# Optimization experiments

Hardware: AMD Instinct MI355X
Metric: run time of the kernel (lower is better)

Reference implementation:

```python
import jax, jax.numpy as jnp
import numpy as np

B, DX, DY, H, K = 16384, 128, 128, 2048, 16
MIN_BIN = 1e-3   # min bin width/height (nflows convention)
MIN_DERIV = 1e-3  # min knot derivative


def setup_inputs() -> dict:
    key = jax.random.key(0)
    k0, k1, k2, k3 = jax.random.split(key, 4)
    x = jax.random.normal(k0, (B, DX), jnp.float32)
    y = jax.random.uniform(k1, (B, DY), jnp.float32, minval=1e-4, maxval=1.0 - 1e-4)
    W1 = jax.random.normal(k2, (DX, H), jnp.float32) / np.sqrt(DX).astype(np.float32)
    b1 = jnp.zeros((H,), jnp.float32)
    W2 = jax.random.normal(k3, (H, DY * (3 * K + 1)), jnp.float32) / np.sqrt(H).astype(np.float32)
    b2 = jnp.zeros((DY * (3 * K + 1),), jnp.float32)
    return {"x": x, "y": y, "W1": W1, "b1": b1, "W2": W2, "b2": b2}


def _rq_spline(y, pdf):
    # y: [B, D] in (0,1); pdf: [B, D, 3K+1] unnormalized spline params
    w_un, h_un, d_un = pdf[..., :K], pdf[..., K:2 * K], pdf[..., 2 * K:]
    widths = MIN_BIN + (1.0 - K * MIN_BIN) * jax.nn.softmax(w_un, axis=-1)   # [B,D,K]
    heights = MIN_BIN + (1.0 - K * MIN_BIN) * jax.nn.softmax(h_un, axis=-1)  # [B,D,K]
    derivs = MIN_DERIV + jax.nn.softplus(d_un)                               # [B,D,K+1]

    pad = [(0, 0), (0, 0), (1, 0)]
    cw = jnp.pad(jnp.cumsum(widths, axis=-1), pad)    # knot x-positions [B,D,K+1]
    ch = jnp.pad(jnp.cumsum(heights, axis=-1), pad)   # knot y-positions [B,D,K+1]

    # data-dependent bin lookup (searchsorted equivalent, vectorized)
    idx = jnp.clip(jnp.sum(y[..., None] >= cw, axis=-1) - 1, 0, K - 1)  # [B,D]
    g = lambda a: jnp.take_along_axis(a, idx[..., None], axis=-1)[..., 0]
    xk, yk = g(cw), g(ch)
    wk, hk = g(widths), g(heights)
    dk = g(derivs)
    dk1 = jnp.take_along_axis(derivs, idx[..., None] + 1, axis=-1)[..., 0]

    s = hk / wk                      # bin slope
    t = (y - xk) / wk                # theta in [0,1]
    omt = 1.0 - t
    denom = s + (dk1 + dk - 2.0 * s) * t * omt
    out = yk + hk * (s * t * t + dk * t * omt) / denom
    deriv = s * s * (dk1 * t * t + 2.0 * s * t * omt + dk * omt * omt) / (denom * denom)
    dlogp = jnp.sum(jnp.log(deriv), axis=-1, keepdims=True)  # [B,1]
    return out, dlogp


def reference(x, y, W1, b1, W2, b2):
    # conditioner MLP: x -> spline params
    h = jax.nn.relu(x @ W1 + b1)
    pdf = (h @ W2 + b2).reshape(x.shape[0], DY, 3 * K + 1)
    return _rq_spline(y, pdf)
```

## Files before the change

kernel.cpp:

```cpp
#include <hip/hip_runtime.h>
#include <hip/hip_fp16.h>
#include <cstdint>
#include <cstddef>

#define B_ROWS 16384
#define DX 128
#define DYDIM 128
#define HDIM 2048
#define NPARAM 49
#define NCOL 6272
#define NTILES 26
#define W2PROWS (NTILES * 256)

typedef __attribute__((ext_vector_type(8))) _Float16 half8v;
typedef __attribute__((ext_vector_type(4))) float f32x4;

__global__ void k_f32_to_f16(const float* __restrict__ in, _Float16* __restrict__ out, int n) {
  int i = blockIdx.x * 256 + threadIdx.x;
  if (i < n) out[i] = (_Float16)in[i];
}

__global__ void k_transpose_f16(const float* __restrict__ in, _Float16* __restrict__ out, int R, int C) {
  __shared__ float tile[32][33];
  int c0 = blockIdx.x * 32, r0 = blockIdx.y * 32;
  int tx = threadIdx.x;
  for (int i = threadIdx.y; i < 32; i += 8)
    tile[i][tx] = in[(size_t)(r0 + i) * C + c0 + tx];
  __syncthreads();
  for (int i = threadIdx.y; i < 32; i += 8)
    out[(size_t)(c0 + i) * R + r0 + tx] = (_Float16)tile[tx][i];
}

__global__ void k_transpose_perm(const float* __restrict__ in, _Float16* __restrict__ out) {
  __shared__ float tile[32][33];
  int c0 = blockIdx.x * 32, r0 = blockIdx.y * 32;
  int tx = threadIdx.x;
  for (int i = threadIdx.y; i < 32; i += 8)
    tile[i][tx] = in[(size_t)(r0 + i) * NCOL + c0 + tx];
  __syncthreads();
  for (int i = threadIdx.y; i < 32; i += 8) {
    int g = c0 + i;
    int t = g / 245;
    int cc = g - t * 245;
    out[(size_t)(t * 256 + cc) * HDIM + r0 + tx] = (_Float16)tile[tx][i];
  }
}

__global__ __launch_bounds__(256) void k_gemm1(
    const _Float16* __restrict__ A, const _Float16* __restrict__ Bt,
    const float* __restrict__ bias, _Float16* __restrict__ C,
    int M, int N, int K) {
  __shared__ _Float16 Abuf[128 * 32];
  __shared__ _Float16 Bbuf[128 * 32];
  const int t = threadIdx.x;
  const int l = t & 63;
  const int w = t >> 6;
  int bx = blockIdx.x, by = blockIdx.y;
  {
    const int nx = gridDim.x;
    const int nwg = nx * gridDim.y;
    const int lin = by * nx + bx;
    const int cpx = nwg >> 3;
    const int sw = (lin & 7) * cpx + (lin >> 3);
    bx = sw % nx;
    by = sw / nx;
  }
  const int tileM = by * 128;
  const int tileN = bx * 128;
  const int wm = w >> 1, wn = w & 1;
  const int srow = w * 16 + (l >> 2);
  const int skel = (l & 3) * 8;
  const char* Ag = (const char*)(A + (size_t)(tileM + srow) * K + skel);
  const char* Bg = (const char*)(Bt + (size_t)(tileN + srow) * K + skel);
  const size_t gRowStep = (size_t)64 * K * 2;
  auto ldsA = (__attribute__((address_space(3))) char*)Abuf;
  auto ldsB = (__attribute__((address_space(3))) char*)Bbuf;
  const int ldsBase = w * 1024;
  f32x4 acc[4][4];
#pragma unroll
  for (int i = 0; i < 4; ++i)
#pragma unroll
    for (int j = 0; j < 4; ++j) acc[i][j] = (f32x4){0.f, 0.f, 0.f, 0.f};
  const int nk = K >> 5;
#define STAGE1(kt)                                                                             \
  do {                                                                                         \
    size_t koff = (size_t)(kt) * 64;                                                           \
    __builtin_amdgcn_global_load_lds(                                                          \
        (const __attribute__((address_space(1))) uint32_t*)(Ag + koff),                        \
        (__attribute__((address_space(3))) uint32_t*)(ldsA + ldsBase), 16, 0, 0);              \
    __builtin_amdgcn_global_load_lds(                                                          \
        (const __attribute__((address_space(1))) uint32_t*)(Ag + koff + gRowStep),             \
        (__attribute__((address_space(3))) uint32_t*)(ldsA + 4096 + ldsBase), 16, 0, 0);       \
    __builtin_amdgcn_global_load_lds(                                                          \
        (const __attribute__((address_space(1))) uint32_t*)(Bg + koff),                        \
        (__attribute__((address_space(3))) uint32_t*)(ldsB + ldsBase), 16, 0, 0);              \
    __builtin_amdgcn_global_load_lds(                                                          \
        (const __attribute__((address_space(1))) uint32_t*)(Bg + koff + gRowStep),             \
        (__attribute__((address_space(3))) uint32_t*)(ldsB + 4096 + ldsBase), 16, 0, 0);       \
  } while (0)
  STAGE1(0);
  const int abase = (wm * 64 + (l & 15)) * 32 + (l >> 4) * 8;
  const int bbase = (wn * 64 + (l & 15)) * 32 + (l >> 4) * 8;
  for (int kt = 0; kt < nk; ++kt) {
    __syncthreads();
    half8v av[4], bv[4];
#pragma unroll
    for (int mf = 0; mf < 4; ++mf)
      av[mf] = *(const half8v*)((const _Float16*)Abuf + abase + mf * 512);
#pragma unroll
    for (int nf = 0; nf < 4; ++nf)
      bv[nf] = *(const half8v*)((const _Float16*)Bbuf + bbase + nf * 512);
#pragma unroll
    for (int mf = 0; mf < 4; ++mf)
#pragma unroll
      for (int nf = 0; nf < 4; ++nf)
        acc[mf][nf] = __builtin_amdgcn_mfma_f32_16x16x32_f16(av[mf], bv[nf], acc[mf][nf], 0, 0, 0);
    __syncthreads();
    if (kt + 1 < nk) STAGE1(kt + 1);
  }
#undef STAGE1
  const int crow0 = tileM + wm * 64 + (l >> 4) * 4;
  const int ccol0 = tileN + wn * 64 + (l & 15);
#pragma unroll
  for (int nf = 0; nf < 4; ++nf) {
    const int col = ccol0 + nf * 16;
    const float bvv = bias[col];
#pragma unroll
    for (int mf = 0; mf < 4; ++mf) {
#pragma unroll
      for (int j = 0; j < 4; ++j) {
        const int row = crow0 + mf * 16 + j;
        float v = fmaxf(acc[mf][nf][j] + bvv, 0.f);
        C[(size_t)row * N + col] = (_Float16)v;
      }
    }
  }
}

__global__ __launch_bounds__(512, 2) void k_gemm2s(
    const _Float16* __restrict__ A, const _Float16* __restrict__ Bt,
    const float* __restrict__ bias, const float* __restrict__ y,
    float* __restrict__ outp, float* __restrict__ gpart, int M) {
  constexpr int K = HDIM;
  constexpr int K2 = K * 2;
  constexpr int NT = K / 64;
  constexpr int ITERS = NT / 2;

  __shared__ char smem[131072];
  __shared__ float red[512];

  const int t = threadIdx.x;
  const int l = t & 63;
  const int w = t >> 6;
  const int wm = w >> 2;
  const int wn = w & 3;
  const int rlo = l & 15;
  const int khi = l >> 4;
  const int wOff = w * 1024;

  int bx = blockIdx.x, by = blockIdx.y;
  {
    const int nx = gridDim.x;
    const int nwg = nx * gridDim.y;
    const int lin = by * nx + bx;
    const int cpx = nwg >> 3;
    const int sw = (lin & 7) * cpx + (lin >> 3);
    bx = sw % nx;
    by = sw / nx;
  }
  const int tileM = by * 256;
  const int tileN = bx * 256;

  int rowj[2], kbj[2];
#pragma unroll
  for (int j = 0; j < 2; ++j) {
    const int phys = j * 8192 + t * 16;
    const int b = phys ^ (((phys >> 9) & 1) << 5);
    rowj[j] = ((b >> 11) << 4) + ((b >> 6) & 15);
    kbj[j] = (((b >> 10) & 1) << 6) + (b & 63);
  }
  const char* pA[2][2];
  const char* pB[2][2];
#pragma unroll
  for (int half = 0; half < 2; ++half)
#pragma unroll
    for (int j = 0; j < 2; ++j) {
      pA[half][j] = (const char*)A + (size_t)(tileM + half * 128 + rowj[j]) * K2 + kbj[j];
      pB[half][j] = (const char*)Bt + (size_t)(tileN + half * 128 + rowj[j]) * K2 + kbj[j];
    }

  auto lds3 = (__attribute__((address_space(3))) char*)smem;

#define LDSA(d, half) ((d) * 32768 + (half) * 16384)
#define LDSB(d, half) (65536 + (d) * 32768 + (half) * 16384)
#define GLDS(srcp, ldsoff)                                                                   \
  __builtin_amdgcn_global_load_lds(                                                           \
      (const __attribute__((address_space(1))) uint32_t*)(srcp),                              \
      (__attribute__((address_space(3))) uint32_t*)(lds3 + (ldsoff) + wOff), 16, 0, 0)
#define STG(op, d, half, kt)                                                                  \
  do {                                                                                        \
    GLDS(p##op[half][0] + (size_t)(kt) * 128, LDS##op(d, half));                              \
    GLDS(p##op[half][1] + (size_t)(kt) * 128, LDS##op(d, half) + 8192);                       \
  } while (0)
#define VM(n) asm volatile("s_waitcnt vmcnt(" #n ")" ::: "memory")
#define NOSTG ((void)0)
#define NOW ((void)0)
#define CFENCE asm volatile("" ::: "memory")

  const int swz = (rlo & 8) ? 32 : 0;
  const int lane16 = rlo * 64 + ((khi * 16) ^ swz);
  const int aW = wm * 8192 + lane16;
  const int bW = 65536 + wn * 4096 + lane16;

  half8v b000, b001, b010, b011, b100, b101, b110, b111;
  f32x4 acc[8][4];
#pragma unroll
  for (int i = 0; i < 8; ++i)
#pragma unroll
    for (int j = 0; j < 4; ++j) acc[i][j] = (f32x4){0.f, 0.f, 0.f, 0.f};

#define MF(fi, gj, av, bv) \
  acc[fi][gj] = __builtin_amdgcn_mfma_f32_16x16x32_f16(av, bv, acc[fi][gj], 0, 0, 0)

#define PHX(d, q, LOADB, WAITS, ...)                                                          \
  do {                                                                                        \
    const int aB = (d) * 32768 + ((q) >> 1) * 16384 + ((q) & 1) * 4096 + aW;                  \
    half8v a00 = *(const half8v*)(smem + aB);                                                 \
    half8v a01 = *(const half8v*)(smem + aB + 1024);                                          \
    half8v a10 = *(const half8v*)(smem + aB + 2048);                                          \
    half8v a11 = *(const half8v*)(smem + aB + 3072);                                          \
    if (LOADB) {                                                                              \
      const int bB = (d) * 32768 + bW;                                                        \
      b000 = *(const half8v*)(smem + bB);                                                     \
      b001 = *(const half8v*)(smem + bB + 1024);                                              \
      b010 = *(const half8v*)(smem + bB + 2048);                                              \
      b011 = *(const half8v*)(smem + bB + 3072);                                              \
      b100 = *(const half8v*)(smem + bB + 16384);                                             \
      b101 = *(const half8v*)(smem + bB + 17408);                                             \
      b110 = *(const half8v*)(smem + bB + 18432);                                             \
      b111 = *(const half8v*)(smem + bB + 19456);                                             \
    }                                                                                         \
    __VA_ARGS__;                                                                              \
    WAITS;                                                                                    \
    CFENCE;                                                                                   \
    __builtin_amdgcn_s_barrier();                                                             \
    CFENCE;                                                                                   \
    __builtin_amdgcn_s_setprio(1);                                                            \
    {                                                                                         \
      constexpr int f0 = ((q) >> 1) * 4 + ((q) & 1) * 2;                                      \
      MF(f0 + 0, 0, a00, b000); MF(f0 + 0, 0, a01, b001);                                     \
      MF(f0 + 0, 1, a00, b010); MF(f0 + 0, 1, a01, b011);                                     \
      MF(f0 + 0, 2, a00, b100); MF(f0 + 0, 2, a01, b101);                                     \
      MF(f0 + 0, 3, a00, b110); MF(f0 + 0, 3, a01, b111);                                     \
      MF(f0 + 1, 0, a10, b000); MF(f0 + 1, 0, a11, b001);                                     \
      MF(f0 + 1, 1, a10, b010); MF(f0 + 1, 1, a11, b011);                                     \
      MF(f0 + 1, 2, a10, b100); MF(f0 + 1, 2, a11, b101);                                     \
      MF(f0 + 1, 3, a10, b110); MF(f0 + 1, 3, a11, b111);                                     \
    }                                                                                         \
    __builtin_amdgcn_s_setprio(0);                                                            \
    CFENCE;                                                                                   \
    __builtin_amdgcn_s_barrier();                                                             \
  } while (0)

  STG(B, 0, 0, 0);
  STG(B, 0, 1, 0);
  STG(A, 0, 0, 0);
  STG(A, 0, 1, 0);
  STG(B, 1, 0, 1);
  STG(B, 1, 1, 1);
  STG(A, 1, 0, 1);
  VM(6);
  CFENCE;
  __builtin_amdgcn_s_barrier();

  for (int it = 0; it < ITERS - 1; ++it) {
    const int kt = 2 * it;
    PHX(0, 0, 1, NOW, STG(A, 1, 1, kt + 1));
    PHX(0, 1, 0, NOW, STG(B, 0, 0, kt + 2));
    PHX(0, 2, 0, NOW, STG(B, 0, 1, kt + 2); STG(A, 0, 0, kt + 2));
    PHX(0, 3, 0, VM(8), NOSTG);
    PHX(1, 0, 1, NOW, STG(A, 0, 1, kt + 2));
    PHX(1, 1, 0, VM(10), STG(B, 1, 0, kt + 3));
    PHX(1, 2, 0, NOW, STG(B, 1, 1, kt + 3); STG(A, 1, 0, kt + 3));
    PHX(1, 3, 0, VM(6), NOSTG);
  }
  PHX(0, 0, 1, NOW, STG(A, 1, 1, NT - 1));
  PHX(0, 1, 0, NOW, NOSTG);
  PHX(0, 2, 0, NOW, NOSTG);
  PHX(0, 3, 0, VM(2), NOSTG);
  PHX(1, 0, 1, NOW, NOSTG);
  PHX(1, 1, 0, VM(0), NOSTG);
  PHX(1, 2, 0, NOW, NOSTG);
  PHX(1, 3, 0, NOW, NOSTG);

#undef PHX
#undef MF
#undef STG
#undef GLDS
#undef LDSA
#undef LDSB

  const int RCt = (bx < 25) ? 245 : 147;
  const int nd  = (bx < 25) ? 5 : 3;

#pragma unroll
  for (int fi = 0; fi < 8; ++fi) {
    const int r0l = (((fi >> 2) * 2 + wm) << 6) + ((fi & 3) << 4) + khi * 4;
#pragma unroll
    for (int gj = 0; gj < 4; ++gj) {
      const int c = (((gj >> 1) * 4 + wn) << 5) + ((gj & 1) << 4) + rlo;
      if (c < RCt) {
        const float bvv = bias[245 * bx + c];
#pragma unroll
        for (int j = 0; j < 4; ++j) {
          const int r = r0l + j;
          *(_Float16*)(smem + r * 512 + ((2 * c) ^ ((r & 31) << 4))) =
              (_Float16)(acc[fi][gj][j] + bvv);
        }
      }
    }
  }
  __syncthreads();

  float lsum = 0.f;
#pragma unroll
  for (int pass = 0; pass < 3; ++pass) {
    const int task = pass * 512 + t;
    const int d = task >> 8;
    const int r = task & 255;
    if (d < nd) {
      const int rbase = r * 512;
      const int rswz = (r & 31) << 4;
      const int cb = 2 * (d * 49);
#define LQ(j) ((float)*(const _Float16*)(smem + rbase + ((cb + 2 * (j)) ^ rswz)))
      float mw = -1e30f, mh = -1e30f;
#pragma unroll
      for (int j = 0; j < 16; ++j) {
        mw = fmaxf(mw, LQ(j));
        mh = fmaxf(mh, LQ(16 + j));
      }
      float sw2 = 0.f, sh = 0.f;
#pragma unroll
      for (int j = 0; j < 16; ++j) {
        sw2 += __expf(LQ(j) - mw);
        sh += __expf(LQ(16 + j) - mh);
      }
      const float rw = 0.984f / sw2, rh = 0.984f / sh;
      const int rg = tileM + r;
      const int dg = 5 * bx + d;
      const float yv = y[(size_t)rg * DYDIM + dg];

      float cws = 0.f, chs = 0.f, xk = 0.f, yk = 0.f, wk = 1.f, hk = 1.f;
      int idx = 0;
#pragma unroll
      for (int j = 0; j < 16; ++j) {
        float wj = 0.001f + rw * __expf(LQ(j) - mw);
        float hj = 0.001f + rh * __expf(LQ(16 + j) - mh);
        if (yv >= cws) { idx = j; xk = cws; yk = chs; wk = wj; hk = hj; }
        cws += wj;
        chs += hj;
      }
      const float du0 = LQ(32 + idx), du1 = LQ(33 + idx);
      const float dk  = 0.001f + fmaxf(du0, 0.f) + log1pf(__expf(-fabsf(du0)));
      const float dk1 = 0.001f + fmaxf(du1, 0.f) + log1pf(__expf(-fabsf(du1)));

      const float s = hk / wk;
      const float tt = (yv - xk) / wk;
      const float omt = 1.f - tt;
      const float dnm = s + (dk1 + dk - 2.f * s) * tt * omt;
      const float o = yk + hk * (s * tt * tt + dk * tt * omt) / dnm;
      const float dr = s * s * (dk1 * tt * tt + 2.f * s * tt * omt + dk * omt * omt) / (dnm * dnm);

      outp[(size_t)rg * DYDIM + dg] = o;
      lsum += __logf(dr);
#undef LQ
    }
  }
  red[t] = lsum;
  __syncthreads();
  if (t < 256)
    gpart[(size_t)bx * B_ROWS + (tileM + t)] = red[t] + red[t + 256];
}

__global__ void k_dlogp_reduce(const float* __restrict__ gpart, float* __restrict__ dlogp) {
  int b = blockIdx.x * 256 + threadIdx.x;
  float s = 0.f;
  for (int tt = 0; tt < NTILES; ++tt) s += gpart[(size_t)tt * B_ROWS + b];
  dlogp[b] = s;
}

extern "C" void kernel_launch(void* const* d_in, const int* in_sizes, int n_in,
                              void* d_out, int out_size, void* d_ws, size_t ws_size,
                              hipStream_t stream) {
  const float* x  = (const float*)d_in[0];
  const float* y  = (const float*)d_in[1];
  const float* W1 = (const float*)d_in[2];
  const float* b1 = (const float*)d_in[3];
  const float* W2 = (const float*)d_in[4];
  const float* b2 = (const float*)d_in[5];
  float* out = (float*)d_out;
  float* dlogp = out + (size_t)B_ROWS * DYDIM;

  char* ws = (char*)d_ws;
  _Float16* w2p = (_Float16*)ws;
  _Float16* h   = w2p + (size_t)W2PROWS * HDIM;
  _Float16* xb  = h + (size_t)B_ROWS * HDIM;
  _Float16* w1t = xb + (size_t)B_ROWS * DX;
  float* gpart  = (float*)(w1t + (size_t)HDIM * DX);

  k_f32_to_f16<<<(B_ROWS * DX + 255) / 256, 256, 0, stream>>>(x, xb, B_ROWS * DX);
  k_transpose_f16<<<dim3(HDIM / 32, DX / 32), dim3(32, 8), 0, stream>>>(W1, w1t, DX, HDIM);
  k_transpose_perm<<<dim3(NCOL / 32, HDIM / 32), dim3(32, 8), 0, stream>>>(W2, w2p);

  k_gemm1<<<dim3(HDIM / 128, B_ROWS / 128), 256, 0, stream>>>(
      xb, w1t, b1, h, B_ROWS, HDIM, DX);

  k_gemm2s<<<dim3(NTILES, B_ROWS / 256), 512, 0, stream>>>(
      h, w2p, b2, y, out, gpart, B_ROWS);

  k_dlogp_reduce<<<B_ROWS / 256, 256, 0, stream>>>(gpart, dlogp);
}
```

Measured before the change: 502.7 us.

## Transpose epilogue LDS layout, remap XCD tile order, reorder MFMA issue

Stores the biased GEMM2 output tile into LDS column-major with packed 32-bit half pairs, so each thread reading a spline parameter column hits consecutive rows across lanes. Spline parameters are loaded once into registers, which removes the repeated LDS reads for the softmax max, sum and bin search, and the y loads are hoisted ahead of the loop. The workgroup-to-tile mapping is hardcoded so each XCD gets 8 contiguous row tiles for L2 reuse, and the MFMA issue order is changed to reuse A fragments. Holding the parameters in registers raises register pressure, and the hardcoded mapping assumes the exact 26x64 grid.

New measurement: 489.9 us. 1.03x faster.

```diff
diff --git a/kernel.cpp b/kernel.cpp
--- a/kernel.cpp
+++ b/kernel.cpp
@@ -160,13 +160,11 @@
 
   int bx = blockIdx.x, by = blockIdx.y;
   {
-    const int nx = gridDim.x;
-    const int nwg = nx * gridDim.y;
-    const int lin = by * nx + bx;
-    const int cpx = nwg >> 3;
-    const int sw = (lin & 7) * cpx + (lin >> 3);
-    bx = sw % nx;
-    by = sw / nx;
+    const int lin = by * 26 + bx;
+    const int xcd = lin & 7;
+    const int slot = lin >> 3;
+    bx = slot >> 3;
+    by = xcd * 8 + (slot & 7);
   }
   const int tileM = by * 256;
   const int tileN = bx * 256;
@@ -248,14 +246,14 @@
     __builtin_amdgcn_s_setprio(1);                                                            \
     {                                                                                         \
       constexpr int f0 = ((q) >> 1) * 4 + ((q) & 1) * 2;                                      \
-      MF(f0 + 0, 0, a00, b000); MF(f0 + 0, 0, a01, b001);                                     \
-      MF(f0 + 0, 1, a00, b010); MF(f0 + 0, 1, a01, b011);                                     \
-      MF(f0 + 0, 2, a00, b100); MF(f0 + 0, 2, a01, b101);                                     \
-      MF(f0 + 0, 3, a00, b110); MF(f0 + 0, 3, a01, b111);                                     \
-      MF(f0 + 1, 0, a10, b000); MF(f0 + 1, 0, a11, b001);                                     \
-      MF(f0 + 1, 1, a10, b010); MF(f0 + 1, 1, a11, b011);                                     \
-      MF(f0 + 1, 2, a10, b100); MF(f0 + 1, 2, a11, b101);                                     \
-      MF(f0 + 1, 3, a10, b110); MF(f0 + 1, 3, a11, b111);                                     \
+      MF(f0 + 0, 0, a00, b000); MF(f0 + 0, 1, a00, b010);                                     \
+      MF(f0 + 0, 2, a00, b100); MF(f0 + 0, 3, a00, b110);                                     \
+      MF(f0 + 1, 0, a10, b000); MF(f0 + 1, 1, a10, b010);                                     \
+      MF(f0 + 1, 2, a10, b100); MF(f0 + 1, 3, a10, b110);                                     \
+      MF(f0 + 0, 0, a01, b001); MF(f0 + 0, 1, a01, b011);                                     \
+      MF(f0 + 0, 2, a01, b101); MF(f0 + 0, 3, a01, b111);                                     \
+      MF(f0 + 1, 0, a11, b001); MF(f0 + 1, 1, a11, b011);                                     \
+      MF(f0 + 1, 2, a11, b101); MF(f0 + 1, 3, a11, b111);                                     \
     }                                                                                         \
     __builtin_amdgcn_s_setprio(0);                                                            \
     CFENCE;                                                                                   \
@@ -311,56 +309,69 @@
       const int c = (((gj >> 1) * 4 + wn) << 5) + ((gj & 1) << 4) + rlo;
       if (c < RCt) {
         const float bvv = bias[245 * bx + c];
-#pragma unroll
-        for (int j = 0; j < 4; ++j) {
-          const int r = r0l + j;
-          *(_Float16*)(smem + r * 512 + ((2 * c) ^ ((r & 31) << 4))) =
-              (_Float16)(acc[fi][gj][j] + bvv);
+        const int cb = c * 512;
+        const int cs = (c & 31) << 4;
+#pragma unroll
+        for (int jp = 0; jp < 2; ++jp) {
+          const int r = r0l + jp * 2;
+          const unsigned short lo =
+              __builtin_bit_cast(unsigned short, (_Float16)(acc[fi][gj][jp * 2] + bvv));
+          const unsigned short hi =
+              __builtin_bit_cast(unsigned short, (_Float16)(acc[fi][gj][jp * 2 + 1] + bvv));
+          *(uint32_t*)(smem + cb + ((2 * r) ^ cs)) = (uint32_t)lo | ((uint32_t)hi << 16);
         }
       }
     }
   }
   __syncthreads();
 
+  const int r = t & 255;
+  const int rg = tileM + r;
+  float yv_[3];
+#pragma unroll
+  for (int pass = 0; pass < 3; ++pass) {
+    const int d = pass * 2 + (t >> 8);
+    yv_[pass] = (d < nd) ? y[(size_t)rg * DYDIM + 5 * bx + d] : 0.f;
+  }
+
+#define LDC(p) ((float)*(const _Float16*)(smem + (size_t)(dD * 49 + (p)) * 512 + \
+                                          ((2 * r) ^ (((dD * 49 + (p)) & 31) << 4))))
   float lsum = 0.f;
 #pragma unroll
   for (int pass = 0; pass < 3; ++pass) {
-    const int task = pass * 512 + t;
-    const int d = task >> 8;
-    const int r = task & 255;
-    if (d < nd) {
-      const int rbase = r * 512;
-      const int rswz = (r & 31) << 4;
-      const int cb = 2 * (d * 49);
-#define LQ(j) ((float)*(const _Float16*)(smem + rbase + ((cb + 2 * (j)) ^ rswz)))
-      float mw = -1e30f, mh = -1e30f;
-#pragma unroll
-      for (int j = 0; j < 16; ++j) {
-        mw = fmaxf(mw, LQ(j));
-        mh = fmaxf(mh, LQ(16 + j));
-      }
+    const int dD = pass * 2 + (t >> 8);
+    if (dD < nd) {
+      float qw[16], qh[16], qd[17];
+#pragma unroll
+      for (int p = 0; p < 16; ++p) { qw[p] = LDC(p); qh[p] = LDC(16 + p); }
+#pragma unroll
+      for (int p = 0; p < 17; ++p) qd[p] = LDC(32 + p);
+
+      float mw = qw[0], mh = qh[0];
+#pragma unroll
+      for (int p = 1; p < 16; ++p) { mw = fmaxf(mw, qw[p]); mh = fmaxf(mh, qh[p]); }
+      float ew[16], eh[16];
       float sw2 = 0.f, sh = 0.f;
 #pragma unroll
-      for (int j = 0; j < 16; ++j) {
-        sw2 += __expf(LQ(j) - mw);
-        sh += __expf(LQ(16 + j) - mh);
+      for (int p = 0; p < 16; ++p) {
+        ew[p] = __expf(qw[p] - mw);
+        eh[p] = __expf(qh[p] - mh);
+        sw2 += ew[p];
+        sh += eh[p];
       }
       const float rw = 0.984f / sw2, rh = 0.984f / sh;
-      const int rg = tileM + r;
-      const int dg = 5 * bx + d;
-      const float yv = y[(size_t)rg * DYDIM + dg];
+      const float yv = yv_[pass];
 
       float cws = 0.f, chs = 0.f, xk = 0.f, yk = 0.f, wk = 1.f, hk = 1.f;
-      int idx = 0;
+      float du0 = qd[0], du1 = qd[1];
 #pragma unroll
       for (int j = 0; j < 16; ++j) {
-        float wj = 0.001f + rw * __expf(LQ(j) - mw);
-        float hj = 0.001f + rh * __expf(LQ(16 + j) - mh);
-        if (yv >= cws) { idx = j; xk = cws; yk = chs; wk = wj; hk = hj; }
+        float wj = 0.001f + rw * ew[j];
+        float hj = 0.001f + rh * eh[j];
+        if (yv >= cws) { xk = cws; yk = chs; wk = wj; hk = hj; du0 = qd[j]; du1 = qd[j + 1]; }
         cws += wj;
         chs += hj;
       }
-      const float du0 = LQ(32 + idx), du1 = LQ(33 + idx);
       const float dk  = 0.001f + fmaxf(du0, 0.f) + log1pf(__expf(-fabsf(du0)));
       const float dk1 = 0.001f + fmaxf(du1, 0.f) + log1pf(__expf(-fabsf(du1)));
 
@@ -371,11 +382,11 @@
       const float o = yk + hk * (s * tt * tt + dk * tt * omt) / dnm;
       const float dr = s * s * (dk1 * tt * tt + 2.f * s * tt * omt + dk * omt * omt) / (dnm * dnm);
 
-      outp[(size_t)rg * DYDIM + dg] = o;
+      outp[(size_t)rg * DYDIM + 5 * bx + dD] = o;
       lsum += __logf(dr);
-#undef LQ
     }
   }
+#undef LDC
   red[t] = lsum;
   __syncthreads();
   if (t < 256)
```
